# Kernel tuning notes

Hardware: AMD Instinct MI355X
Metric: run time of the kernel (lower is better)

Reference implementation:

```python
import jax, jax.numpy as jnp
import numpy as np

N_NODES = 20000
N_EDGES = 160000
EPS = 1e-5
LEAKY_SLOPE = 0.01


def gcn_conv(x, src, dst, W, b, num_nodes):
    """PyG GCNConv: self-loops + symmetric normalization. out = D^-1/2 A_hat D^-1/2 (x W) + b."""
    h = x @ W  # [N, out]
    loop = jnp.arange(num_nodes, dtype=src.dtype)
    s = jnp.concatenate([src, loop])
    d = jnp.concatenate([dst, loop])
    deg = jax.ops.segment_sum(jnp.ones_like(d, dtype=h.dtype), d, num_segments=num_nodes)
    dinv = jnp.where(deg > 0, jax.lax.rsqrt(jnp.maximum(deg, 1.0)) * jnp.where(deg > 0, 1.0, 0.0), 0.0)
    norm = dinv[s] * dinv[d]  # [E+N]
    msgs = h[s] * norm[:, None]  # gather + scale (memory-bound)
    out = jax.ops.segment_sum(msgs, d, num_segments=num_nodes)
    return out + b


def setup_inputs() -> dict:
    key = jax.random.key(0)
    ks = jax.random.split(key, 8)
    x = jax.random.normal(ks[0], (N_NODES, 1), dtype=jnp.float32)
    edge_index = jax.random.randint(ks[1], (2, N_EDGES), 0, N_NODES, dtype=jnp.int32)
    s = 0.02
    W1 = jax.random.normal(ks[2], (1, 2048), dtype=jnp.float32) * s
    b1 = jnp.zeros((2048,), jnp.float32)
    W2 = jax.random.normal(ks[3], (2048, 1024), dtype=jnp.float32) * s
    b2 = jnp.zeros((1024,), jnp.float32)
    gamma = jnp.ones((1024,), jnp.float32)
    beta = jnp.zeros((1024,), jnp.float32)
    running_mean = jnp.zeros((1024,), jnp.float32)
    running_var = jnp.ones((1024,), jnp.float32)
    lW1 = jax.random.normal(ks[4], (1024, 256), dtype=jnp.float32) * s
    lb1 = jnp.zeros((256,), jnp.float32)
    lW2 = jax.random.normal(ks[5], (256, 124), dtype=jnp.float32) * s
    lb2 = jnp.zeros((124,), jnp.float32)
    return dict(x=x, edge_index=edge_index, W1=W1, b1=b1, W2=W2, b2=b2,
                gamma=gamma, beta=beta, running_mean=running_mean,
                running_var=running_var, lW1=lW1, lb1=lb1, lW2=lW2, lb2=lb2)


def reference(x, edge_index, W1, b1, W2, b2, gamma, beta,
              running_mean, running_var, lW1, lb1, lW2, lb2):
    n = x.shape[0]
    src, dst = edge_index[0], edge_index[1]
    h = gcn_conv(x, src, dst, W1, b1, n)          # GCNConv(1, 2048); dropout is identity in eval
    h = gcn_conv(h, src, dst, W2, b2, n)          # GCNConv(2048, 1024)
    h = (h - running_mean) * (gamma * jax.lax.rsqrt(running_var + EPS)) + beta  # BatchNorm (eval)
    h = h @ lW1 + lb1                              # Linear 1024->256
    h = jnp.where(h >= 0, h, LEAKY_SLOPE * h)      # LeakyReLU
    h = h @ lW2 + lb2                              # Linear 256->124
    return jax.nn.log_softmax(h, axis=1)
```

## Files before the change

### kernel.cpp

```cpp
#include <hip/hip_runtime.h>
#include <math.h>

#define N_NODES 20000
#define N_EDGES 160000
#define EPSB 1e-5f
#define SLOPE 0.01f

typedef __attribute__((ext_vector_type(8))) short short8;
typedef __attribute__((ext_vector_type(4))) float f32x4;

#define OFF_DEG    0
#define OFF_A1     20000
#define OFF_CN     40000
#define OFF_A2     60000
#define OFF_V      80000
#define OFF_U      81024
#define OFF_R      82048
#define OFF_RU     82304
#define OFF_S      82560
#define OFF_ZEND   82816
#define OFF_BFRAG  82816

#define T_STRIDE 264

__device__ __forceinline__ unsigned short f2bf(float f) {
    unsigned u = __float_as_uint(f);
    return (unsigned short)((u + 0x7FFFu + ((u >> 16) & 1u)) >> 16);
}

__global__ void E1_deg_v_bf(const int* __restrict__ dst, int* __restrict__ deg,
                            const float* __restrict__ W1, const float* __restrict__ b1,
                            const float* __restrict__ W2, const float* __restrict__ lW2,
                            float* __restrict__ v, float* __restrict__ u,
                            unsigned short* __restrict__ bfrag) {
    int b = blockIdx.x;
    if (b < 625) {
        int e = b * 256 + threadIdx.x;
        atomicAdd(&deg[dst[e]], 1);
    } else if (b < 881) {
        int bb = b - 625;
        int k  = (bb & 3) * 256 + threadIdx.x;
        int c0 = (bb >> 2) * 32;
        float av = 0.f, au = 0.f;
        for (int c = c0; c < c0 + 32; ++c) {
            float w = W2[c * 1024 + k];
            av = fmaf(W1[c], w, av);
            au = fmaf(b1[c], w, au);
        }
        atomicAdd(&v[k], av);
        atomicAdd(&u[k], au);
    } else {
        int i = (b - 881) * 256 + threadIdx.x;
        int ct = i >> 9, ks = (i >> 6) & 7, lane = i & 63;
        int n  = ct * 16 + (lane & 15);
        int kb = ks * 32 + (lane >> 4) * 8;
        union { unsigned short u8[8]; short8 v8; } pk;
#pragma unroll
        for (int j = 0; j < 8; ++j)
            pk.u8[j] = (n < 124) ? f2bf(lW2[(kb + j) * 124 + n]) : (unsigned short)0;
        ((short8*)bfrag)[i] = pk.v8;
    }
}

__global__ void E2_edges1_rs(const int* __restrict__ src, const int* __restrict__ dst,
                             const int* __restrict__ deg, const float* __restrict__ x,
                             float* __restrict__ a1, float* __restrict__ cn,
                             const float* __restrict__ v, const float* __restrict__ u,
                             const float* __restrict__ gamma, const float* __restrict__ beta,
                             const float* __restrict__ mean, const float* __restrict__ var,
                             const float* __restrict__ b2, const float* __restrict__ lW1,
                             const float* __restrict__ lb1,
                             float* __restrict__ r, float* __restrict__ ru, float* __restrict__ s) {
    int b = blockIdx.x;
    if (b < 625) {
        int e = b * 256 + threadIdx.x;
        int sn = src[e], d = dst[e];
        float nrm = rsqrtf((float)((deg[sn] + 1) * (deg[d] + 1)));
        atomicAdd(&a1[d], nrm * x[sn]);
        atomicAdd(&cn[d], nrm);
    } else {
        int bb = b - 625, m = threadIdx.x, k0 = bb * 32;
        float ar = 0.f, aru = 0.f, as = 0.f;
        for (int k = k0; k < k0 + 32; ++k) {
            float g = gamma[k] * rsqrtf(var[k] + EPSB);
            float w = lW1[k * 256 + m];
            ar  = fmaf(v[k] * g, w, ar);
            aru = fmaf(u[k] * g, w, aru);
            as  = fmaf(fmaf(b2[k] - mean[k], g, beta[k]), w, as);
        }
        if (bb == 0) as += lb1[m];
        atomicAdd(&r[m], ar);
        atomicAdd(&ru[m], aru);
        atomicAdd(&s[m], as);
    }
}

__global__ void E3_edges2(const int* __restrict__ src, const int* __restrict__ dst,
                          const int* __restrict__ deg, const float* __restrict__ x,
                          const float* __restrict__ a1, float* __restrict__ a2) {
    int e = blockIdx.x * 256 + threadIdx.x;
    int sn = src[e], d = dst[e];
    float i_s = 1.f / (float)(deg[sn] + 1);
    float dd  = rsqrtf((float)(deg[d] + 1));
    float a1f = fmaf(i_s, x[sn], a1[sn]);
    atomicAdd(&a2[d], sqrtf(i_s) * dd * a1f);
}

__global__ __launch_bounds__(256, 2) void F_final(
    const int* __restrict__ deg, const float* __restrict__ x,
    const float* __restrict__ a1, const float* __restrict__ cn,
    const float* __restrict__ a2,
    const float* __restrict__ r, const float* __restrict__ ru,
    const float* __restrict__ s,
    const short8* __restrict__ bfrag, const float* __restrict__ lb2,
    float* __restrict__ out) {
    __shared__ unsigned short tsh[16 * T_STRIDE];
    __shared__ float a_sh[16], cn_sh[16];
    __shared__ float logits[16 * 132];
    int tid  = threadIdx.x;
    int lane = tid & 63;
    int wave = __builtin_amdgcn_readfirstlane(tid >> 6);
    int row  = lane & 15, quad = lane >> 4;

    short8 bf0[8], bf1[8];
#pragma unroll
    for (int ks = 0; ks < 8; ++ks) {
        bf0[ks] = bfrag[((wave * 2 + 0) * 8 + ks) * 64 + lane];
        bf1[ks] = bfrag[((wave * 2 + 1) * 8 + ks) * 64 + lane];
    }
    float cr = r[tid], cu = ru[tid], cs = s[tid];

    for (int it = 0; it < 2; ++it) {
        int node0 = (blockIdx.x * 2 + it) * 16;
        if (tid < 16) {
            int n = node0 + tid;
            float d2  = 1.f / (float)(deg[n] + 1);
            float a1f = fmaf(d2, x[n], a1[n]);
            a_sh[tid]  = fmaf(d2, a1f, a2[n]);
            cn_sh[tid] = cn[n] + d2;
        }
        __syncthreads();

#pragma unroll
        for (int n = 0; n < 16; ++n) {
            float t = fmaf(cn_sh[n], cu, fmaf(a_sh[n], cr, cs));
            t = fmaf(SLOPE, fminf(t, 0.f), fmaxf(t, 0.f));
            tsh[n * T_STRIDE + tid] = f2bf(t);
        }
        __syncthreads();

        f32x4 acc0 = {0.f, 0.f, 0.f, 0.f}, acc1 = {0.f, 0.f, 0.f, 0.f};
        const unsigned short* tb = &tsh[row * T_STRIDE + quad * 8];
#pragma unroll
        for (int ks = 0; ks < 8; ++ks) {
            short8 af = *(const short8*)(tb + ks * 32);
            acc0 = __builtin_amdgcn_mfma_f32_16x16x32_bf16(af, bf0[ks], acc0, 0, 0, 0);
            acc1 = __builtin_amdgcn_mfma_f32_16x16x32_bf16(af, bf1[ks], acc1, 0, 0, 0);
        }
        int colbase = wave * 32;
#pragma unroll
        for (int rg = 0; rg < 4; ++rg) {
            int rw = quad * 4 + rg;
            logits[rw * 132 + colbase + row]      = acc0[rg];
            logits[rw * 132 + colbase + 16 + row] = acc1[rg];
        }
        __syncthreads();

        int nd = tid >> 4, sub = tid & 15, c0 = sub * 8;
        int jend = 124 - c0; if (jend > 8) jend = 8;
        float vbuf[8];
        const float* lrow = &logits[nd * 132 + c0];
        float mx = -1e30f;
        for (int j = 0; j < jend; ++j) {
            vbuf[j] = lrow[j] + lb2[c0 + j];
            mx = fmaxf(mx, vbuf[j]);
        }
        mx = fmaxf(mx, __shfl_xor(mx, 1, 16));
        mx = fmaxf(mx, __shfl_xor(mx, 2, 16));
        mx = fmaxf(mx, __shfl_xor(mx, 4, 16));
        mx = fmaxf(mx, __shfl_xor(mx, 8, 16));
        float sm = 0.f;
        for (int j = 0; j < jend; ++j) sm += __expf(vbuf[j] - mx);
        sm += __shfl_xor(sm, 1, 16);
        sm += __shfl_xor(sm, 2, 16);
        sm += __shfl_xor(sm, 4, 16);
        sm += __shfl_xor(sm, 8, 16);
        float lz = mx + __logf(sm);
        float* orow = out + (node0 + nd) * 124 + c0;
        for (int j = 0; j < jend; ++j) orow[j] = vbuf[j] - lz;
    }
}

extern "C" void kernel_launch(void* const* d_in, const int* in_sizes, int n_in,
                              void* d_out, int out_size, void* d_ws, size_t ws_size,
                              hipStream_t stream) {
    const float* x     = (const float*)d_in[0];
    const int*   ei    = (const int*)d_in[1];
    const int*   src   = ei;
    const int*   dst   = ei + N_EDGES;
    const float* W1    = (const float*)d_in[2];
    const float* b1    = (const float*)d_in[3];
    const float* W2    = (const float*)d_in[4];
    const float* b2    = (const float*)d_in[5];
    const float* gamma = (const float*)d_in[6];
    const float* beta  = (const float*)d_in[7];
    const float* rmean = (const float*)d_in[8];
    const float* rvar  = (const float*)d_in[9];
    const float* lW1   = (const float*)d_in[10];
    const float* lb1   = (const float*)d_in[11];
    const float* lW2   = (const float*)d_in[12];
    const float* lb2   = (const float*)d_in[13];
    float* out = (float*)d_out;
    float* ws  = (float*)d_ws;

    int*   deg = (int*)(ws + OFF_DEG);
    float* a1  = ws + OFF_A1;
    float* cn  = ws + OFF_CN;
    float* a2  = ws + OFF_A2;
    float* v   = ws + OFF_V;
    float* u   = ws + OFF_U;
    float* r   = ws + OFF_R;
    float* ru  = ws + OFF_RU;
    float* s   = ws + OFF_S;
    unsigned short* bfrag = (unsigned short*)(ws + OFF_BFRAG);

    hipMemsetAsync(ws, 0, OFF_ZEND * sizeof(float), stream);

    E1_deg_v_bf<<<625 + 256 + 16, 256, 0, stream>>>(dst, deg, W1, b1, W2, lW2, v, u, bfrag);
    E2_edges1_rs<<<625 + 32, 256, 0, stream>>>(src, dst, deg, x, a1, cn, v, u, gamma, beta,
                                               rmean, rvar, b2, lW1, lb1, r, ru, s);
    E3_edges2<<<625, 256, 0, stream>>>(src, dst, deg, x, a1, a2);
    F_final<<<625, 256, 0, stream>>>(deg, x, a1, cn, a2, r, ru, s,
                                     (const short8*)bfrag, lb2, out);
}
```

Before: 153.3 us.

## Factor edge normalization into per-node prescaled values and use unsafe float atomics

Edge normalization is factored into per-node terms. New node-parallel kernels precompute dinv*x and dinv (and later a second-hop prescaled value), so the edge kernels only gather one value per edge and scatter-add it. No per-edge degree lookups or rsqrt remain. All float atomics switch to unsafeAtomicAdd, which lets the hardware use fast float atomic instructions. The cost is two extra small kernel launches and more workspace.

```diff
diff --git a/kernel.cpp b/kernel.cpp
--- a/kernel.cpp
+++ b/kernel.cpp
@@ -10,16 +10,17 @@
 typedef __attribute__((ext_vector_type(4))) float f32x4;
 
 #define OFF_DEG    0
-#define OFF_A1     20000
-#define OFF_CN     40000
-#define OFF_A2     60000
+#define OFF_ACC2   20000
+#define OFF_B      60000
 #define OFF_V      80000
 #define OFF_U      81024
 #define OFF_R      82048
 #define OFF_RU     82304
 #define OFF_S      82560
 #define OFF_ZEND   82816
-#define OFF_BFRAG  82816
+#define OFF_Q1     82816
+#define OFF_Q2     122816
+#define OFF_BFRAG  142816
 
 #define T_STRIDE 264
 
@@ -28,7 +29,7 @@
     return (unsigned short)((u + 0x7FFFu + ((u >> 16) & 1u)) >> 16);
 }
 
-__global__ void E1_deg_v_bf(const int* __restrict__ dst, int* __restrict__ deg,
+__global__ void K1_deg_v_bf(const int* __restrict__ dst, int* __restrict__ deg,
                             const float* __restrict__ W1, const float* __restrict__ b1,
                             const float* __restrict__ W2, const float* __restrict__ lW2,
                             float* __restrict__ v, float* __restrict__ u,
@@ -47,8 +48,8 @@
             av = fmaf(W1[c], w, av);
             au = fmaf(b1[c], w, au);
         }
-        atomicAdd(&v[k], av);
-        atomicAdd(&u[k], au);
+        unsafeAtomicAdd(&v[k], av);
+        unsafeAtomicAdd(&u[k], au);
     } else {
         int i = (b - 881) * 256 + threadIdx.x;
         int ct = i >> 9, ks = (i >> 6) & 7, lane = i & 63;
@@ -62,24 +63,24 @@
     }
 }
 
-__global__ void E2_edges1_rs(const int* __restrict__ src, const int* __restrict__ dst,
-                             const int* __restrict__ deg, const float* __restrict__ x,
-                             float* __restrict__ a1, float* __restrict__ cn,
-                             const float* __restrict__ v, const float* __restrict__ u,
-                             const float* __restrict__ gamma, const float* __restrict__ beta,
-                             const float* __restrict__ mean, const float* __restrict__ var,
-                             const float* __restrict__ b2, const float* __restrict__ lW1,
-                             const float* __restrict__ lb1,
-                             float* __restrict__ r, float* __restrict__ ru, float* __restrict__ s) {
+__global__ void K2_q1_rs(const int* __restrict__ deg, const float* __restrict__ x,
+                         float2* __restrict__ q1,
+                         const float* __restrict__ v, const float* __restrict__ u,
+                         const float* __restrict__ gamma, const float* __restrict__ beta,
+                         const float* __restrict__ mean, const float* __restrict__ var,
+                         const float* __restrict__ b2, const float* __restrict__ lW1,
+                         const float* __restrict__ lb1,
+                         float* __restrict__ r, float* __restrict__ ru, float* __restrict__ s) {
     int b = blockIdx.x;
-    if (b < 625) {
-        int e = b * 256 + threadIdx.x;
-        int sn = src[e], d = dst[e];
-        float nrm = rsqrtf((float)((deg[sn] + 1) * (deg[d] + 1)));
-        atomicAdd(&a1[d], nrm * x[sn]);
-        atomicAdd(&cn[d], nrm);
+    if (b < 79) {
+        int n = b * 256 + threadIdx.x;
+        if (n < N_NODES) {
+            float dinv = rsqrtf((float)(deg[n] + 1));
+            float2 q; q.x = dinv * x[n]; q.y = dinv;
+            q1[n] = q;
+        }
     } else {
-        int bb = b - 625, m = threadIdx.x, k0 = bb * 32;
+        int bb = b - 79, m = threadIdx.x, k0 = bb * 32;
         float ar = 0.f, aru = 0.f, as = 0.f;
         for (int k = k0; k < k0 + 32; ++k) {
             float g = gamma[k] * rsqrtf(var[k] + EPSB);
@@ -89,27 +90,41 @@
             as  = fmaf(fmaf(b2[k] - mean[k], g, beta[k]), w, as);
         }
         if (bb == 0) as += lb1[m];
-        atomicAdd(&r[m], ar);
-        atomicAdd(&ru[m], aru);
-        atomicAdd(&s[m], as);
-    }
-}
-
-__global__ void E3_edges2(const int* __restrict__ src, const int* __restrict__ dst,
-                          const int* __restrict__ deg, const float* __restrict__ x,
-                          const float* __restrict__ a1, float* __restrict__ a2) {
+        unsafeAtomicAdd(&r[m], ar);
+        unsafeAtomicAdd(&ru[m], aru);
+        unsafeAtomicAdd(&s[m], as);
+    }
+}
+
+__global__ void K3_edges1(const int* __restrict__ src, const int* __restrict__ dst,
+                          const float2* __restrict__ q1, float* __restrict__ acc2) {
     int e = blockIdx.x * 256 + threadIdx.x;
     int sn = src[e], d = dst[e];
-    float i_s = 1.f / (float)(deg[sn] + 1);
-    float dd  = rsqrtf((float)(deg[d] + 1));
-    float a1f = fmaf(i_s, x[sn], a1[sn]);
-    atomicAdd(&a2[d], sqrtf(i_s) * dd * a1f);
+    float2 q = q1[sn];
+    unsafeAtomicAdd(&acc2[2 * d],     q.x);
+    unsafeAtomicAdd(&acc2[2 * d + 1], q.y);
+}
+
+__global__ void K4_q2(const float2* __restrict__ q1, const float2* __restrict__ acc2,
+                      float* __restrict__ q2) {
+    int n = blockIdx.x * 256 + threadIdx.x;
+    if (n < N_NODES) {
+        float2 q  = q1[n];
+        float2 ac = acc2[n];
+        float agg1f = q.y * (ac.x + q.x);
+        q2[n] = q.y * agg1f;
+    }
+}
+
+__global__ void K5_edges2(const int* __restrict__ src, const int* __restrict__ dst,
+                          const float* __restrict__ q2, float* __restrict__ B) {
+    int e = blockIdx.x * 256 + threadIdx.x;
+    unsafeAtomicAdd(&B[dst[e]], q2[src[e]]);
 }
 
 __global__ __launch_bounds__(256, 2) void F_final(
-    const int* __restrict__ deg, const float* __restrict__ x,
-    const float* __restrict__ a1, const float* __restrict__ cn,
-    const float* __restrict__ a2,
+    const float2* __restrict__ q1, const float* __restrict__ q2,
+    const float* __restrict__ B, const float2* __restrict__ acc2,
     const float* __restrict__ r, const float* __restrict__ ru,
     const float* __restrict__ s,
     const short8* __restrict__ bfrag, const float* __restrict__ lb2,
@@ -134,10 +149,10 @@
         int node0 = (blockIdx.x * 2 + it) * 16;
         if (tid < 16) {
             int n = node0 + tid;
-            float d2  = 1.f / (float)(deg[n] + 1);
-            float a1f = fmaf(d2, x[n], a1[n]);
-            a_sh[tid]  = fmaf(d2, a1f, a2[n]);
-            cn_sh[tid] = cn[n] + d2;
+            float2 q = q1[n];
+            float dinv = q.y;
+            a_sh[tid]  = dinv * (B[n] + q2[n]);
+            cn_sh[tid] = dinv * (acc2[n].y + dinv);
         }
         __syncthreads();
 
@@ -213,23 +228,26 @@
     float* out = (float*)d_out;
     float* ws  = (float*)d_ws;
 
-    int*   deg = (int*)(ws + OFF_DEG);
-    float* a1  = ws + OFF_A1;
-    float* cn  = ws + OFF_CN;
-    float* a2  = ws + OFF_A2;
-    float* v   = ws + OFF_V;
-    float* u   = ws + OFF_U;
-    float* r   = ws + OFF_R;
-    float* ru  = ws + OFF_RU;
-    float* s   = ws + OFF_S;
+    int*    deg  = (int*)(ws + OFF_DEG);
+    float*  acc2 = ws + OFF_ACC2;
+    float*  B    = ws + OFF_B;
+    float*  v    = ws + OFF_V;
+    float*  u    = ws + OFF_U;
+    float*  r    = ws + OFF_R;
+    float*  ru   = ws + OFF_RU;
+    float*  s    = ws + OFF_S;
+    float2* q1   = (float2*)(ws + OFF_Q1);
+    float*  q2   = ws + OFF_Q2;
     unsigned short* bfrag = (unsigned short*)(ws + OFF_BFRAG);
 
     hipMemsetAsync(ws, 0, OFF_ZEND * sizeof(float), stream);
 
-    E1_deg_v_bf<<<625 + 256 + 16, 256, 0, stream>>>(dst, deg, W1, b1, W2, lW2, v, u, bfrag);
-    E2_edges1_rs<<<625 + 32, 256, 0, stream>>>(src, dst, deg, x, a1, cn, v, u, gamma, beta,
-                                               rmean, rvar, b2, lW1, lb1, r, ru, s);
-    E3_edges2<<<625, 256, 0, stream>>>(src, dst, deg, x, a1, a2);
-    F_final<<<625, 256, 0, stream>>>(deg, x, a1, cn, a2, r, ru, s,
-                                     (const short8*)bfrag, lb2, out);
-}
+    K1_deg_v_bf<<<625 + 256 + 16, 256, 0, stream>>>(dst, deg, W1, b1, W2, lW2, v, u, bfrag);
+    K2_q1_rs<<<79 + 32, 256, 0, stream>>>(deg, x, q1, v, u, gamma, beta,
+                                          rmean, rvar, b2, lW1, lb1, r, ru, s);
+    K3_edges1<<<625, 256, 0, stream>>>(src, dst, q1, acc2);
+    K4_q2<<<79, 256, 0, stream>>>(q1, (const float2*)acc2, q2);
+    K5_edges2<<<625, 256, 0, stream>>>(src, dst, q2, B);
+    F_final<<<625, 256, 0, stream>>>(q1, q2, B, (const float2*)acc2,
+                                     r, ru, s, (const short8*)bfrag, lb2, out);
+}
```

Result: slower. 159.3 us (+3.9%).

## Pack per-node x, degree and edge accumulators into float4 and use unsafe atomics

Applied to the files above, without the earlier changes.

Per-node state (x, float degree, first-layer sum, norm sum) is interleaved into one float4 array so each edge does a single vectorized gather instead of several scattered loads. The normalization algebra is refactored so the destination-side factors are applied later in the final kernel, which removes the per-edge reads of the destination degree. Atomics switch to unsafeAtomicAdd so hardware float atomics can be used. The degree is now counted in float, and there is an extra copy pass for x plus a larger zeroed workspace.

```diff
diff --git a/kernel.cpp b/kernel.cpp
--- a/kernel.cpp
+++ b/kernel.cpp
@@ -9,17 +9,15 @@
 typedef __attribute__((ext_vector_type(8))) short short8;
 typedef __attribute__((ext_vector_type(4))) float f32x4;
 
-#define OFF_DEG    0
-#define OFF_A1     20000
-#define OFF_CN     40000
-#define OFF_A2     60000
-#define OFF_V      80000
-#define OFF_U      81024
-#define OFF_R      82048
-#define OFF_RU     82304
-#define OFF_S      82560
-#define OFF_ZEND   82816
-#define OFF_BFRAG  82816
+#define OFF_ND     0
+#define OFF_B      80000
+#define OFF_V      100000
+#define OFF_U      101024
+#define OFF_R      102048
+#define OFF_RU     102304
+#define OFF_S      102560
+#define OFF_ZEND   102816
+#define OFF_BFRAG  102816
 
 #define T_STRIDE 264
 
@@ -28,7 +26,8 @@
     return (unsigned short)((u + 0x7FFFu + ((u >> 16) & 1u)) >> 16);
 }
 
-__global__ void E1_deg_v_bf(const int* __restrict__ dst, int* __restrict__ deg,
+__global__ void E1_deg_v_bf(const int* __restrict__ dst, float* __restrict__ ndf,
+                            const float* __restrict__ x,
                             const float* __restrict__ W1, const float* __restrict__ b1,
                             const float* __restrict__ W2, const float* __restrict__ lW2,
                             float* __restrict__ v, float* __restrict__ u,
@@ -36,7 +35,7 @@
     int b = blockIdx.x;
     if (b < 625) {
         int e = b * 256 + threadIdx.x;
-        atomicAdd(&deg[dst[e]], 1);
+        unsafeAtomicAdd(&ndf[4 * dst[e] + 1], 1.0f);
     } else if (b < 881) {
         int bb = b - 625;
         int k  = (bb & 3) * 256 + threadIdx.x;
@@ -47,9 +46,9 @@
             av = fmaf(W1[c], w, av);
             au = fmaf(b1[c], w, au);
         }
-        atomicAdd(&v[k], av);
-        atomicAdd(&u[k], au);
-    } else {
+        unsafeAtomicAdd(&v[k], av);
+        unsafeAtomicAdd(&u[k], au);
+    } else if (b < 897) {
         int i = (b - 881) * 256 + threadIdx.x;
         int ct = i >> 9, ks = (i >> 6) & 7, lane = i & 63;
         int n  = ct * 16 + (lane & 15);
@@ -59,25 +58,29 @@
         for (int j = 0; j < 8; ++j)
             pk.u8[j] = (n < 124) ? f2bf(lW2[(kb + j) * 124 + n]) : (unsigned short)0;
         ((short8*)bfrag)[i] = pk.v8;
+    } else {
+        int n = (b - 897) * 256 + threadIdx.x;
+        if (n < N_NODES) ndf[4 * n] = x[n];
     }
 }
 
 __global__ void E2_edges1_rs(const int* __restrict__ src, const int* __restrict__ dst,
-                             const int* __restrict__ deg, const float* __restrict__ x,
-                             float* __restrict__ a1, float* __restrict__ cn,
+                             float* __restrict__ ndf,
                              const float* __restrict__ v, const float* __restrict__ u,
                              const float* __restrict__ gamma, const float* __restrict__ beta,
                              const float* __restrict__ mean, const float* __restrict__ var,
                              const float* __restrict__ b2, const float* __restrict__ lW1,
                              const float* __restrict__ lb1,
-                             float* __restrict__ r, float* __restrict__ ru, float* __restrict__ s) {
+                             float* __restrict__ r, float* __restrict__ ru,
+                             float* __restrict__ s) {
     int b = blockIdx.x;
     if (b < 625) {
         int e = b * 256 + threadIdx.x;
         int sn = src[e], d = dst[e];
-        float nrm = rsqrtf((float)((deg[sn] + 1) * (deg[d] + 1)));
-        atomicAdd(&a1[d], nrm * x[sn]);
-        atomicAdd(&cn[d], nrm);
+        float2 sv = ((const float2*)ndf)[2 * sn];
+        float dinv = rsqrtf(sv.y + 1.0f);
+        unsafeAtomicAdd(&ndf[4 * d + 2], dinv * sv.x);
+        unsafeAtomicAdd(&ndf[4 * d + 3], dinv);
     } else {
         int bb = b - 625, m = threadIdx.x, k0 = bb * 32;
         float ar = 0.f, aru = 0.f, as = 0.f;
@@ -89,27 +92,24 @@
             as  = fmaf(fmaf(b2[k] - mean[k], g, beta[k]), w, as);
         }
         if (bb == 0) as += lb1[m];
-        atomicAdd(&r[m], ar);
-        atomicAdd(&ru[m], aru);
-        atomicAdd(&s[m], as);
+        unsafeAtomicAdd(&r[m], ar);
+        unsafeAtomicAdd(&ru[m], aru);
+        unsafeAtomicAdd(&s[m], as);
     }
 }
 
 __global__ void E3_edges2(const int* __restrict__ src, const int* __restrict__ dst,
-                          const int* __restrict__ deg, const float* __restrict__ x,
-                          const float* __restrict__ a1, float* __restrict__ a2) {
+                          const float4* __restrict__ nd4, float* __restrict__ B) {
     int e = blockIdx.x * 256 + threadIdx.x;
     int sn = src[e], d = dst[e];
-    float i_s = 1.f / (float)(deg[sn] + 1);
-    float dd  = rsqrtf((float)(deg[d] + 1));
-    float a1f = fmaf(i_s, x[sn], a1[sn]);
-    atomicAdd(&a2[d], sqrtf(i_s) * dd * a1f);
+    float4 nv = nd4[sn];
+    float dinv = rsqrtf(nv.y + 1.0f);
+    float q2 = dinv * dinv * (nv.z + dinv * nv.x);
+    unsafeAtomicAdd(&B[d], q2);
 }
 
 __global__ __launch_bounds__(256, 2) void F_final(
-    const int* __restrict__ deg, const float* __restrict__ x,
-    const float* __restrict__ a1, const float* __restrict__ cn,
-    const float* __restrict__ a2,
+    const float4* __restrict__ nd4, const float* __restrict__ B,
     const float* __restrict__ r, const float* __restrict__ ru,
     const float* __restrict__ s,
     const short8* __restrict__ bfrag, const float* __restrict__ lb2,
@@ -134,10 +134,11 @@
         int node0 = (blockIdx.x * 2 + it) * 16;
         if (tid < 16) {
             int n = node0 + tid;
-            float d2  = 1.f / (float)(deg[n] + 1);
-            float a1f = fmaf(d2, x[n], a1[n]);
-            a_sh[tid]  = fmaf(d2, a1f, a2[n]);
-            cn_sh[tid] = cn[n] + d2;
+            float4 nv = nd4[n];
+            float dinv = rsqrtf(nv.y + 1.0f);
+            float q2n  = dinv * dinv * (nv.z + dinv * nv.x);
+            a_sh[tid]  = dinv * (B[n] + q2n);
+            cn_sh[tid] = dinv * (nv.w + dinv);
         }
         __syncthreads();
 
@@ -213,10 +214,8 @@
     float* out = (float*)d_out;
     float* ws  = (float*)d_ws;
 
-    int*   deg = (int*)(ws + OFF_DEG);
-    float* a1  = ws + OFF_A1;
-    float* cn  = ws + OFF_CN;
-    float* a2  = ws + OFF_A2;
+    float* ndf = ws + OFF_ND;
+    float* B   = ws + OFF_B;
     float* v   = ws + OFF_V;
     float* u   = ws + OFF_U;
     float* r   = ws + OFF_R;
@@ -226,10 +225,11 @@
 
     hipMemsetAsync(ws, 0, OFF_ZEND * sizeof(float), stream);
 
-    E1_deg_v_bf<<<625 + 256 + 16, 256, 0, stream>>>(dst, deg, W1, b1, W2, lW2, v, u, bfrag);
-    E2_edges1_rs<<<625 + 32, 256, 0, stream>>>(src, dst, deg, x, a1, cn, v, u, gamma, beta,
+    E1_deg_v_bf<<<625 + 256 + 16 + 79, 256, 0, stream>>>(dst, ndf, x, W1, b1, W2, lW2,
+                                                         v, u, bfrag);
+    E2_edges1_rs<<<625 + 32, 256, 0, stream>>>(src, dst, ndf, v, u, gamma, beta,
                                                rmean, rvar, b2, lW1, lb1, r, ru, s);
-    E3_edges2<<<625, 256, 0, stream>>>(src, dst, deg, x, a1, a2);
-    F_final<<<625, 256, 0, stream>>>(deg, x, a1, cn, a2, r, ru, s,
+    E3_edges2<<<625, 256, 0, stream>>>(src, dst, (const float4*)ndf, B);
+    F_final<<<625, 256, 0, stream>>>((const float4*)ndf, B, r, ru, s,
                                      (const short8*)bfrag, lb2, out);
 }
```

After: 156.7 us. 2.2% more time.
